# Optimization experiments

Measured on AMD Instinct MI355X. Metric: run time of the kernel, lower is better.

## Reference

```python
import jax, jax.numpy as jnp
import numpy as np

DIM = 1024
HEADS = 16
DIM_HEAD = 64
INNER = HEADS * DIM_HEAD  # 1024
B, N = 2, 2048


def setup_inputs() -> dict:
    key = jax.random.key(0)
    ks = jax.random.split(key, 6)
    x = jax.random.normal(ks[0], (B, N, DIM), dtype=jnp.float32)
    rel_pos_bias = jax.random.normal(ks[1], (1, HEADS, N, N), dtype=jnp.float32)
    g = jnp.ones((DIM,), dtype=jnp.float32)
    # Linear weights stored torch-style as [out_features, in_features].
    # Note: original zero-inits Wo; we use small random values so outputs/grads are non-trivial.
    Wq = jax.random.normal(ks[2], (INNER, DIM), dtype=jnp.float32) * (DIM ** -0.5)
    Wkv = jax.random.normal(ks[3], (2 * INNER, DIM), dtype=jnp.float32) * (DIM ** -0.5)
    Wo = jax.random.normal(ks[4], (DIM, INNER), dtype=jnp.float32) * (INNER ** -0.5)
    return {"x": x, "rel_pos_bias": rel_pos_bias, "g": g, "Wq": Wq, "Wkv": Wkv, "Wo": Wo}


def reference(x, rel_pos_bias, g, Wq, Wkv, Wo):
    eps = 1e-5  # x is float32
    # Faithful to source: normalize over dim=1 (sequence axis), biased variance.
    mean = jnp.mean(x, axis=1, keepdims=True)          # [b, 1, d]
    var = jnp.var(x, axis=1, keepdims=True)            # [b, 1, d]
    xn = (x - mean) * jax.lax.rsqrt(jnp.maximum(var, eps)) * g

    q = xn @ Wq.T                                      # [b, n, inner]
    kv = xn @ Wkv.T                                    # [b, n, 2*inner]
    k, v = jnp.split(kv, 2, axis=-1)

    def to_heads(t):  # b n (h d) -> b h n d
        b, n, _ = t.shape
        return t.reshape(b, n, HEADS, DIM_HEAD).transpose(0, 2, 1, 3)

    q, k, v = to_heads(q), to_heads(k), to_heads(v)
    q = q * (DIM_HEAD ** -0.5)

    sim = jnp.einsum('bhid,bhjd->bhij', q, k) + rel_pos_bias  # [b, h, n, n]
    attn = jax.nn.softmax(sim, axis=-1)
    out = jnp.einsum('bhij,bhjd->bhid', attn, v)              # [b, h, n, d]
    out = out.transpose(0, 2, 1, 3).reshape(x.shape[0], x.shape[1], INNER)
    return out @ Wo.T                                         # [b, n, dim]
```

## Files before the change

### kernel.cpp

```cpp
#include <hip/hip_runtime.h>
#include <hip/hip_bf16.h>

typedef __bf16 bf16;
typedef __attribute__((ext_vector_type(8))) __bf16 bf16x8;
typedef __attribute__((ext_vector_type(4))) __bf16 bf16x4;
typedef __attribute__((ext_vector_type(4))) float f32x4;
typedef __attribute__((ext_vector_type(16))) float f32x16;
typedef __attribute__((ext_vector_type(4))) unsigned int u32x4;

#define DIMD  1024
#define SEQ   2048
#define BATCH 2
#define HEADS 16
#define INNER 1024
#define QKVN  3072
#define ROWS  (BATCH*SEQ)
#define LOG2E 1.44269504f

__global__ void ln_partial(const float* __restrict__ x,
                           float* __restrict__ psum, float* __restrict__ psq) {
    const int nc = blockIdx.x;
    const int b  = blockIdx.y;
    const int t  = threadIdx.x;
    const float* xp = x + ((size_t)b*SEQ + (size_t)nc*32)*DIMD;
    float s0=0,s1=0,s2=0,s3=0,q0=0,q1=0,q2=0,q3=0;
    for (int r=0; r<32; ++r) {
        const float* row = xp + (size_t)r*DIMD;
        float v0=row[t], v1=row[t+256], v2=row[t+512], v3=row[t+768];
        s0+=v0; q0+=v0*v0; s1+=v1; q1+=v1*v1;
        s2+=v2; q2+=v2*v2; s3+=v3; q3+=v3*v3;
    }
    float* ps = psum + ((size_t)b*64 + nc)*DIMD;
    float* pq = psq  + ((size_t)b*64 + nc)*DIMD;
    ps[t]=s0; ps[t+256]=s1; ps[t+512]=s2; ps[t+768]=s3;
    pq[t]=q0; pq[t+256]=q1; pq[t+512]=q2; pq[t+768]=q3;
}

__global__ void ln_finalize(const float* __restrict__ psum, const float* __restrict__ psq,
                            const float* __restrict__ g,
                            float* __restrict__ scale, float* __restrict__ shift) {
    const int d = blockIdx.x*256 + threadIdx.x;
    const int b = blockIdx.y;
    float s=0.f, q=0.f;
    for (int nc=0; nc<64; ++nc) {
        s += psum[((size_t)b*64+nc)*DIMD + d];
        q += psq [((size_t)b*64+nc)*DIMD + d];
    }
    const float inv_n = 1.f/(float)SEQ;
    float mean = s*inv_n;
    float var  = q*inv_n - mean*mean;
    var = fmaxf(var, 1e-5f);
    scale[b*DIMD+d] = g[d]*rsqrtf(var);
    shift[b*DIMD+d] = mean;
}

__global__ void ln_apply(const float* __restrict__ x,
                         const float* __restrict__ scale, const float* __restrict__ shift,
                         bf16* __restrict__ xn) {
    size_t idx = ((size_t)blockIdx.x*256 + threadIdx.x)*4;
    int b = (int)(idx >> 21);
    int d = (int)(idx & (DIMD-1));
    f32x4 v  = *reinterpret_cast<const f32x4*>(x + idx);
    f32x4 sc = *reinterpret_cast<const f32x4*>(scale + (size_t)b*DIMD + d);
    f32x4 sh = *reinterpret_cast<const f32x4*>(shift + (size_t)b*DIMD + d);
    bf16x4 o;
    o.x = (bf16)((v.x - sh.x)*sc.x);
    o.y = (bf16)((v.y - sh.y)*sc.y);
    o.z = (bf16)((v.z - sh.z)*sc.z);
    o.w = (bf16)((v.w - sh.w)*sc.w);
    *reinterpret_cast<bf16x4*>(xn + idx) = o;
}

__global__ void castk_all(const float* __restrict__ Wq, const float* __restrict__ Wkv,
                          const float* __restrict__ Wo,
                          bf16* __restrict__ wqkv, bf16* __restrict__ wo, float qs) {
    int i = (blockIdx.x*256 + threadIdx.x)*4;
    f32x4 v; bf16* dst;
    if (i < 1048576)      { v = *reinterpret_cast<const f32x4*>(Wq + i);
                            v.x*=qs; v.y*=qs; v.z*=qs; v.w*=qs; dst = wqkv + i; }
    else if (i < 3145728) { v = *reinterpret_cast<const f32x4*>(Wkv + (i-1048576));
                            dst = wqkv + i; }
    else                  { v = *reinterpret_cast<const f32x4*>(Wo + (i-3145728));
                            dst = wo + (i-3145728); }
    bf16x4 o; o.x=(bf16)v.x; o.y=(bf16)v.y; o.z=(bf16)v.z; o.w=(bf16)v.w;
    *reinterpret_cast<bf16x4*>(dst) = o;
}

__device__ __forceinline__ void gload16(const void* g, void* l) {
    __builtin_amdgcn_global_load_lds(
        (const __attribute__((address_space(1))) unsigned int*)g,
        (__attribute__((address_space(3))) unsigned int*)l,
        16, 0, 0);
}

__device__ inline void store_out(float* p, float v) { *p = v; }
__device__ inline void store_out(bf16*  p, float v) { *p = (bf16)v; }

template <typename OT, bool FUSE_VT>
__global__ __launch_bounds__(256, 2)
void gemm_bt(const bf16* __restrict__ A, const bf16* __restrict__ B,
             OT* __restrict__ C, bf16* __restrict__ vTout, int M, int N, int K) {
    __shared__ bf16 As[128*64];
    __shared__ bf16 Bs[128*64];
    const int t = threadIdx.x;
    const int wave = t >> 6, lane = t & 63;
    const int wr = wave >> 1, wc = wave & 1;
    const int m0 = blockIdx.y*128, n0 = blockIdx.x*128;
    const int lr = lane & 15, lg = lane >> 4;
    const int srow = wave*32 + (lane>>3);
    const int scol = (lane&7)*8;

    f32x4 acc[4][4];
    #pragma unroll
    for (int i=0;i<4;++i)
        #pragma unroll
        for (int j=0;j<4;++j) acc[i][j] = (f32x4){0.f,0.f,0.f,0.f};

    for (int k0=0; k0<K; k0+=64) {
        #pragma unroll
        for (int i=0;i<4;++i) {
            gload16(A + (size_t)(m0+srow+8*i)*K + k0 + scol, As + (srow+8*i)*64 + scol);
            gload16(B + (size_t)(n0+srow+8*i)*K + k0 + scol, Bs + (srow+8*i)*64 + scol);
        }
        __syncthreads();
        #pragma unroll
        for (int kk=0; kk<2; ++kk) {
            bf16x8 a[4], b[4];
            #pragma unroll
            for (int mi=0;mi<4;++mi)
                a[mi] = *reinterpret_cast<const bf16x8*>(As + (wr*64+mi*16+lr)*64 + kk*32+lg*8);
            #pragma unroll
            for (int ni=0;ni<4;++ni)
                b[ni] = *reinterpret_cast<const bf16x8*>(Bs + (wc*64+ni*16+lr)*64 + kk*32+lg*8);
            #pragma unroll
            for (int mi=0;mi<4;++mi)
                #pragma unroll
                for (int ni=0;ni<4;++ni)
                    acc[mi][ni] = __builtin_amdgcn_mfma_f32_16x16x32_bf16(a[mi], b[ni], acc[mi][ni], 0, 0, 0);
        }
        __syncthreads();
    }
    if (FUSE_VT && n0 >= 2*INNER) {
        #pragma unroll
        for (int mi=0;mi<4;++mi)
            #pragma unroll
            for (int ni=0;ni<4;++ni) {
                int row0 = m0 + wr*64 + mi*16 + lg*4;
                int col  = n0 + wc*64 + ni*16 + lr;
                int vcol = col - 2*INNER;
                int bb = row0 >> 11, nn = row0 & (SEQ-1);
                size_t vrow = (size_t)(bb*HEADS + (vcol>>6))*64 + (vcol&63);
                bf16x4 pk;
                pk[0]=(bf16)acc[mi][ni][0]; pk[1]=(bf16)acc[mi][ni][1];
                pk[2]=(bf16)acc[mi][ni][2]; pk[3]=(bf16)acc[mi][ni][3];
                *reinterpret_cast<bf16x4*>(vTout + vrow*SEQ + nn) = pk;
            }
    } else {
        #pragma unroll
        for (int mi=0;mi<4;++mi)
            #pragma unroll
            for (int ni=0;ni<4;++ni)
                #pragma unroll
                for (int r=0;r<4;++r) {
                    int row = m0 + wr*64 + mi*16 + lg*4 + r;
                    int col = n0 + wc*64 + ni*16 + lr;
                    store_out(&C[(size_t)row*N + col], acc[mi][ni][r]);
                }
    }
}


__device__ __forceinline__ unsigned pk2(float a, float b) {
    union { bf16 h[2]; unsigned u; } x;
    x.h[0] = (bf16)a; x.h[1] = (bf16)b;
    return x.u;
}

#define ATTN_BARRIER()                                         \
    __builtin_amdgcn_sched_barrier(0);                         \
    asm volatile("s_waitcnt lgkmcnt(0)" ::: "memory");         \
    __builtin_amdgcn_s_barrier();                              \
    __builtin_amdgcn_sched_barrier(0)

#define ATTN_ITER(CUR, T)                                                          \
  {                                                                                \
              \
    if ((T)+1 < 32) {                                                              \
      *reinterpret_cast<bf16x8*>(&Ks[0][(CUR)^1][st_off])  = krA;                  \
      *reinterpret_cast<bf16x8*>(&Ks[1][(CUR)^1][st_off])  = krB;                  \
      *reinterpret_cast<bf16x8*>(&VTs[0][(CUR)^1][st_off]) = vrA;                  \
      *reinterpret_cast<bf16x8*>(&VTs[1][(CUR)^1][st_off]) = vrB;                  \
      _Pragma("unroll")                                                            \
      for (int i=0;i<4;++i)                                                        \
        *reinterpret_cast<f32x4*>(&BsL[(CUR)^1][bst[i]]) = breg[i];                \
    }                                                                              \
                      \
    if ((T)+2 < 32) {                                                              \
      krA = *reinterpret_cast<const bf16x8*>(kbase0 + (size_t)(((T)+2)*64+srow)*QKVN + scol);  \
      krB = *reinterpret_cast<const bf16x8*>(kbase1 + (size_t)(((T)+2)*64+srow)*QKVN + scol);  \
      vrA = *reinterpret_cast<const bf16x8*>(vtb0 + (size_t)srow*SEQ + ((T)+2)*64 + scol);     \
      vrB = *reinterpret_cast<const bf16x8*>(vtb1 + (size_t)srow*SEQ + ((T)+2)*64 + scol);     \
      _Pragma("unroll")                                                            \
      for (int i=0;i<4;++i)                                                        \
        breg[i] = *reinterpret_cast<const f32x4*>(bgl + (size_t)(32*i)*SEQ + ((T)+2)*64);      \
    }                                                                              \
                                    \
    f32x16 p0 = (f32x16)(0.0f), p1 = (f32x16)(0.0f);                               \
    __builtin_amdgcn_s_setprio(1);                                                 \
    _Pragma("unroll")                                                              \
    for (int s=0;s<4;++s) {                                                        \
      bf16x8 kf0 = *reinterpret_cast<const bf16x8*>(&myK[(CUR)*4096 + koff[0][s]]); \
      p0 = __builtin_amdgcn_mfma_f32_32x32x16_bf16(kf0, qf[s], p0, 0,0,0);         \
      bf16x8 kf1 = *reinterpret_cast<const bf16x8*>(&myK[(CUR)*4096 + koff[1][s]]); \
      p1 = __builtin_amdgcn_mfma_f32_32x32x16_bf16(kf1, qf[s], p1, 0,0,0);         \
    }                                                                              \
    __builtin_amdgcn_s_setprio(0);                                                 \
                              \
    f32x4 bb0[4], bb1[4];                                                          \
    _Pragma("unroll")                                                              \
    for (int rr=0;rr<4;++rr) {                                                     \
      bb0[rr] = *reinterpret_cast<const f32x4*>(&BsL[CUR][brd[0][rr]]);            \
      bb1[rr] = *reinterpret_cast<const f32x4*>(&BsL[CUR][brd[1][rr]]);            \
    }                                                                              \
            \
    float v0[16], v1[16];                                                          \
    _Pragma("unroll")                                                              \
    for (int r=0;r<16;++r) {                                                       \
      v0[r] = __builtin_fmaf(bb0[r>>2][r&3], LOG2E, p0[r]);                        \
      v1[r] = __builtin_fmaf(bb1[r>>2][r&3], LOG2E, p1[r]);                        \
    }                                                                              \
    float mx[8];                                                                   \
    _Pragma("unroll")                                                              \
    for (int i=0;i<8;++i)                                                          \
      mx[i] = fmaxf(fmaxf(v0[i], v0[i+8]), fmaxf(v1[i], v1[i+8]));                 \
    _Pragma("unroll")                                                              \
    for (int i=0;i<4;++i) mx[i] = fmaxf(mx[i], mx[i+4]);                           \
    float vmax = fmaxf(fmaxf(mx[0],mx[2]), fmaxf(mx[1],mx[3]));                    \
    vmax = fmaxf(vmax, __shfl_xor(vmax, 32));                                      \
    if (!__all(vmax <= m + 11.5f)) {                                               \
      float mnew = fmaxf(m, vmax);                                                 \
      float sc = __builtin_amdgcn_exp2f(m - mnew);                                 \
      m = mnew; l *= sc;                                                           \
      _Pragma("unroll")                                                            \
      for (int r=0;r<16;++r) {                                                     \
        float scr = __shfl(sc, (r&3)+8*(r>>2)+4*hi);                               \
        accO0[r] *= scr; accO1[r] *= scr;                                          \
      }                                                                            \
    }                                                                              \
    float e0[16], e1[16];                                                          \
    _Pragma("unroll")                                                              \
    for (int r=0;r<16;++r) {                                                       \
      e0[r] = __builtin_amdgcn_exp2f(v0[r] - m);                                   \
      e1[r] = __builtin_amdgcn_exp2f(v1[r] - m);                                   \
    }                                                                              \
    float sm[8];                                                                   \
    _Pragma("unroll")                                                              \
    for (int i=0;i<8;++i) sm[i] = (e0[i]+e0[i+8]) + (e1[i]+e1[i+8]);               \
    _Pragma("unroll")                                                              \
    for (int i=0;i<4;++i) sm[i] += sm[i+4];                                        \
    float rsum = (sm[0]+sm[2]) + (sm[1]+sm[3]);                                    \
    rsum += __shfl_xor(rsum, 32);                                                  \
    l += rsum;                                                                     \
           \
    unsigned W0[4][2], W1[4][2];                                                   \
    _Pragma("unroll")                                                              \
    for (int rr=0;rr<4;++rr) {                                                     \
      W0[rr][0] = pk2(e0[4*rr+0], e0[4*rr+1]);                                     \
      W0[rr][1] = pk2(e0[4*rr+2], e0[4*rr+3]);                                     \
      W1[rr][0] = pk2(e1[4*rr+0], e1[4*rr+1]);                                     \
      W1[rr][1] = pk2(e1[4*rr+2], e1[4*rr+3]);                                     \
    }                                                                              \
                               \
    bf16x8 pa[4];                                                                  \
    _Pragma("unroll")                                                              \
    for (int s4=0;s4<4;++s4) {                                                     \
      unsigned u[4];                                                               \
      _Pragma("unroll")                                                            \
      for (int hh=0;hh<2;++hh) {                                                   \
        unsigned a0 = (s4>>1) ? W1[2*(s4&1)  ][hh] : W0[2*(s4&1)  ][hh];           \
        unsigned a1 = (s4>>1) ? W1[2*(s4&1)+1][hh] : W0[2*(s4&1)+1][hh];           \
        unsigned X = hi ? a0 : a1;                                                 \
        unsigned R = (unsigned)__shfl_xor((int)X, 32);                             \
        u[hh]   = hi ? R  : a0;                                                    \
        u[2+hh] = hi ? a1 : R;                                                     \
      }                                                                            \
      u32x4 uv = {u[0], u[1], u[2], u[3]};                                         \
      pa[s4] = __builtin_bit_cast(bf16x8, uv);                                     \
    }                                                                              \
                                                                        \
    __builtin_amdgcn_s_setprio(1);                                                 \
    _Pragma("unroll")                                                              \
    for (int s4=0;s4<4;++s4) {                                                     \
      bf16x8 vfa = *reinterpret_cast<const bf16x8*>(&myV[(CUR)*4096 + voff[0][s4]]); \
      accO0 = __builtin_amdgcn_mfma_f32_32x32x16_bf16(pa[s4], vfa, accO0, 0,0,0);  \
      bf16x8 vfb = *reinterpret_cast<const bf16x8*>(&myV[(CUR)*4096 + voff[1][s4]]); \
      accO1 = __builtin_amdgcn_mfma_f32_32x32x16_bf16(pa[s4], vfb, accO1, 0,0,0);  \
    }                                                                              \
    __builtin_amdgcn_s_setprio(0);                                                 \
    ATTN_BARRIER();                                                                \
  }

__global__ __launch_bounds__(512, 1)
void attn_kernel(const bf16* __restrict__ qkv, const bf16* __restrict__ vTg,
                 const float* __restrict__ bias, bf16* __restrict__ oh) {
    __shared__ bf16 Ks[2][2][64*64];
    __shared__ bf16 VTs[2][2][64*64];
    __shared__ float BsL[2][128*64];

    const int qt = blockIdx.x, h = blockIdx.y;
    const int t = threadIdx.x;
    const int w = t >> 6, lane = t & 63;
    const int wb = w >> 2;
    const int wq = w & 3;
    const int ql = lane & 31, hi = lane >> 5;
    const int q0 = qt*128;

    int koff[2][4], voff[2][4];
    #pragma unroll
    for (int B2=0;B2<2;++B2)
        #pragma unroll
        for (int s=0;s<4;++s) {
            koff[B2][s] = (32*B2+ql)*64 + (((2*s+hi) ^ (ql&7))*8);
            voff[B2][s] = (32*B2+ql)*64 + (((2*s+hi) ^ (ql&7))*8);
        }
    bf16* myK = (bf16*)Ks[wb];
    bf16* myV = (bf16*)VTs[wb];

    int bst[4];
    {
        int rlow = t>>4;
        int swg  = ((t&15) ^ (rlow&15))*4;
        #pragma unroll
        for (int i=0;i<4;++i)
            bst[i] = (32*i + rlow)*64 + swg;
    }
    int brd[2][4];
    #pragma unroll
    for (int B2=0;B2<2;++B2)
        #pragma unroll
        for (int rr=0;rr<4;++rr)
            brd[B2][rr] = (wq*32+ql)*64 + (((8*B2+2*rr+hi) ^ (ql&15))*4);

    const int srow = t>>3;
    const int scol = (t&7)*8;
    const int st_off = srow*64 + (((t&7) ^ (srow&7))*8);

    const bf16* qrow = qkv + ((size_t)(wb*SEQ + q0 + wq*32 + ql))*QKVN + h*64 + hi*8;
    bf16x8 qf[4];
    #pragma unroll
    for (int s=0;s<4;++s)
        qf[s] = *reinterpret_cast<const bf16x8*>(qrow + 16*s);

    const bf16* kbase0 = qkv + INNER + h*64;
    const bf16* kbase1 = qkv + (size_t)SEQ*QKVN + INNER + h*64;
    const bf16* vtb0   = vTg + (size_t)h*64*SEQ;
    const bf16* vtb1   = vTg + (size_t)(HEADS + h)*64*SEQ;
    const float* bgl = bias + ((size_t)h*SEQ + (size_t)(q0 + (t>>4)))*SEQ + 4*(t&15);

    bf16x8 krA, krB, vrA, vrB;
    f32x4 breg[4];

    *reinterpret_cast<bf16x8*>(&Ks[0][0][st_off]) =
        *reinterpret_cast<const bf16x8*>(kbase0 + (size_t)srow*QKVN + scol);
    *reinterpret_cast<bf16x8*>(&Ks[1][0][st_off]) =
        *reinterpret_cast<const bf16x8*>(kbase1 + (size_t)srow*QKVN + scol);
    *reinterpret_cast<bf16x8*>(&VTs[0][0][st_off]) =
        *reinterpret_cast<const bf16x8*>(vtb0 + (size_t)srow*SEQ + scol);
    *reinterpret_cast<bf16x8*>(&VTs[1][0][st_off]) =
        *reinterpret_cast<const bf16x8*>(vtb1 + (size_t)srow*SEQ + scol);
    #pragma unroll
    for (int i=0;i<4;++i)
        breg[i] = *reinterpret_cast<const f32x4*>(bgl + (size_t)(32*i)*SEQ);
    #pragma unroll
    for (int i=0;i<4;++i)
        *reinterpret_cast<f32x4*>(&BsL[0][bst[i]]) = breg[i];
    krA = *reinterpret_cast<const bf16x8*>(kbase0 + (size_t)(64+srow)*QKVN + scol);
    krB = *reinterpret_cast<const bf16x8*>(kbase1 + (size_t)(64+srow)*QKVN + scol);
    vrA = *reinterpret_cast<const bf16x8*>(vtb0 + (size_t)srow*SEQ + 64 + scol);
    vrB = *reinterpret_cast<const bf16x8*>(vtb1 + (size_t)srow*SEQ + 64 + scol);
    #pragma unroll
    for (int i=0;i<4;++i)
        breg[i] = *reinterpret_cast<const f32x4*>(bgl + (size_t)(32*i)*SEQ + 64);
    ATTN_BARRIER();

    float m = -__builtin_inff();
    float l = 0.f;
    f32x16 accO0 = (f32x16)(0.0f), accO1 = (f32x16)(0.0f);

    for (int t2 = 0; t2 < 32; t2 += 2) {
        ATTN_ITER(0, t2);
        ATTN_ITER(1, t2+1);
    }

    float linv = 1.f/l;
    bf16* ob = oh + ((size_t)(wb*SEQ + q0 + wq*32))*INNER + h*64 + ql;
    #pragma unroll
    for (int r=0;r<16;++r) {
        int qoff = (r&3) + 8*(r>>2) + 4*hi;
        float li = __shfl(linv, qoff);
        ob[(size_t)qoff*INNER]      = (bf16)(accO0[r]*li);
        ob[(size_t)qoff*INNER + 32] = (bf16)(accO1[r]*li);
    }
}

extern "C" void kernel_launch(void* const* d_in, const int* in_sizes, int n_in,
                              void* d_out, int out_size, void* d_ws, size_t ws_size,
                              hipStream_t stream) {
    const float* x    = (const float*)d_in[0];
    const float* bias = (const float*)d_in[1];
    const float* g    = (const float*)d_in[2];
    const float* Wq   = (const float*)d_in[3];
    const float* Wkv  = (const float*)d_in[4];
    const float* Wo   = (const float*)d_in[5];
    float* out = (float*)d_out;

    char* ws = (char*)d_ws;
    bf16*  xn    = (bf16*)(ws);
    bf16*  vT    = (bf16*)(ws + 8388608);
    bf16*  wqkv  = (bf16*)(ws + 16777216);
    bf16*  wo    = (bf16*)(ws + 23068672);
    bf16*  qkv   = (bf16*)(ws + 25165824);
    bf16*  oh    = (bf16*)(ws + 50331648);
    float* psum  = (float*)(ws + 58720256);
    float* psq   = (float*)(ws + 59244544);
    float* scale = (float*)(ws + 59768832);
    float* shift = (float*)(ws + 59777024);

    ln_partial <<<dim3(64,2), 256, 0, stream>>>(x, psum, psq);
    ln_finalize<<<dim3(4,2),  256, 0, stream>>>(psum, psq, g, scale, shift);
    ln_apply   <<<dim3(4096), 256, 0, stream>>>(x, scale, shift, xn);

    castk_all<<<dim3(4096), 256, 0, stream>>>(Wq, Wkv, Wo, wqkv, wo, 0.125f*LOG2E);

    gemm_bt<bf16,true><<<dim3(24,32), 256, 0, stream>>>(xn, wqkv, qkv, vT, ROWS, QKVN, DIMD);

    attn_kernel<<<dim3(16,16), 512, 0, stream>>>(qkv, vT, bias, oh);

    gemm_bt<float,false><<<dim3(8,32), 256, 0, stream>>>(oh, wo, out, nullptr, ROWS, INNER, INNER);
}
```

Before: 172.0 us.

## Switch attention K/V/bias staging to direct global-to-LDS loads with triple buffering

Staging of K, V and bias tiles in the attention loop changes from register-staged loads plus LDS stores to direct global-to-LDS loads (gload16). The pre-swizzled source addresses keep the existing LDS layout. K/V get a three-deep buffer ring with loads issued two tiles ahead, and bias is double-buffered one tile ahead. Waits use partial vmcnt counts so loads stay in flight across the barrier. This removes VGPR staging and LDS write instructions from the loop and deepens prefetch, at the cost of more LDS and careful counter-based synchronisation that can race if the counts are wrong.

```diff
diff --git a/kernel.cpp b/kernel.cpp
--- a/kernel.cpp
+++ b/kernel.cpp
@@ -176,51 +176,40 @@
     return x.u;
 }
 
-#define ATTN_BARRIER()                                         \
-    __builtin_amdgcn_sched_barrier(0);                         \
-    asm volatile("s_waitcnt lgkmcnt(0)" ::: "memory");         \
-    __builtin_amdgcn_s_barrier();                              \
-    __builtin_amdgcn_sched_barrier(0)
-
-#define ATTN_ITER(CUR, T)                                                          \
+#define ATTN_ITER(KB, KW, BB, BW, T, TAIL)                                         \
   {                                                                                \
-              \
-    if ((T)+1 < 32) {                                                              \
-      *reinterpret_cast<bf16x8*>(&Ks[0][(CUR)^1][st_off])  = krA;                  \
-      *reinterpret_cast<bf16x8*>(&Ks[1][(CUR)^1][st_off])  = krB;                  \
-      *reinterpret_cast<bf16x8*>(&VTs[0][(CUR)^1][st_off]) = vrA;                  \
-      *reinterpret_cast<bf16x8*>(&VTs[1][(CUR)^1][st_off]) = vrB;                  \
+                         \
+    if (!(TAIL) || (T)+1 < 32) {                                                   \
       _Pragma("unroll")                                                            \
-      for (int i=0;i<4;++i)                                                        \
-        *reinterpret_cast<f32x4*>(&BsL[(CUR)^1][bst[i]]) = breg[i];                \
-    }                                                                              \
-                      \
-    if ((T)+2 < 32) {                                                              \
-      krA = *reinterpret_cast<const bf16x8*>(kbase0 + (size_t)(((T)+2)*64+srow)*QKVN + scol);  \
-      krB = *reinterpret_cast<const bf16x8*>(kbase1 + (size_t)(((T)+2)*64+srow)*QKVN + scol);  \
-      vrA = *reinterpret_cast<const bf16x8*>(vtb0 + (size_t)srow*SEQ + ((T)+2)*64 + scol);     \
-      vrB = *reinterpret_cast<const bf16x8*>(vtb1 + (size_t)srow*SEQ + ((T)+2)*64 + scol);     \
-      _Pragma("unroll")                                                            \
-      for (int i=0;i<4;++i)                                                        \
-        breg[i] = *reinterpret_cast<const f32x4*>(bgl + (size_t)(32*i)*SEQ + ((T)+2)*64);      \
-    }                                                                              \
+      for (int i_=0;i_<4;++i_)                                                     \
+        gload16(bptr + (size_t)(32*i_)*SEQ + ((T)+1)*64, &BsL[BW][t*4 + i_*2048]); \
+    }                                                                              \
+    __builtin_amdgcn_sched_barrier(0);                                             \
+                                                 \
+    if (!(TAIL) || (T)+2 < 32) {                                                   \
+      gload16(kA + (size_t)((T)+2)*64*QKVN, &Ks[0][KW][t*8]);                      \
+      gload16(kB + (size_t)((T)+2)*64*QKVN, &Ks[1][KW][t*8]);                      \
+      gload16(vA + ((T)+2)*64,              &VTs[0][KW][t*8]);                     \
+      gload16(vB + ((T)+2)*64,              &VTs[1][KW][t*8]);                     \
+    }                                                                              \
+    __builtin_amdgcn_sched_barrier(0);                                             \
                                     \
     f32x16 p0 = (f32x16)(0.0f), p1 = (f32x16)(0.0f);                               \
     __builtin_amdgcn_s_setprio(1);                                                 \
     _Pragma("unroll")                                                              \
     for (int s=0;s<4;++s) {                                                        \
-      bf16x8 kf0 = *reinterpret_cast<const bf16x8*>(&myK[(CUR)*4096 + koff[0][s]]); \
+      bf16x8 kf0 = *reinterpret_cast<const bf16x8*>(&myK[(KB)*4096 + koff[0][s]]); \
       p0 = __builtin_amdgcn_mfma_f32_32x32x16_bf16(kf0, qf[s], p0, 0,0,0);         \
-      bf16x8 kf1 = *reinterpret_cast<const bf16x8*>(&myK[(CUR)*4096 + koff[1][s]]); \
+      bf16x8 kf1 = *reinterpret_cast<const bf16x8*>(&myK[(KB)*4096 + koff[1][s]]); \
       p1 = __builtin_amdgcn_mfma_f32_32x32x16_bf16(kf1, qf[s], p1, 0,0,0);         \
     }                                                                              \
     __builtin_amdgcn_s_setprio(0);                                                 \
-                              \
+                                       \
     f32x4 bb0[4], bb1[4];                                                          \
     _Pragma("unroll")                                                              \
     for (int rr=0;rr<4;++rr) {                                                     \
-      bb0[rr] = *reinterpret_cast<const f32x4*>(&BsL[CUR][brd[0][rr]]);            \
-      bb1[rr] = *reinterpret_cast<const f32x4*>(&BsL[CUR][brd[1][rr]]);            \
+      bb0[rr] = *reinterpret_cast<const f32x4*>(&BsL[BB][brd[0][rr]]);             \
+      bb1[rr] = *reinterpret_cast<const f32x4*>(&BsL[BB][brd[1][rr]]);             \
     }                                                                              \
             \
     float v0[16], v1[16];                                                          \
@@ -291,21 +280,26 @@
     __builtin_amdgcn_s_setprio(1);                                                 \
     _Pragma("unroll")                                                              \
     for (int s4=0;s4<4;++s4) {                                                     \
-      bf16x8 vfa = *reinterpret_cast<const bf16x8*>(&myV[(CUR)*4096 + voff[0][s4]]); \
+      bf16x8 vfa = *reinterpret_cast<const bf16x8*>(&myV[(KB)*4096 + voff[0][s4]]); \
       accO0 = __builtin_amdgcn_mfma_f32_32x32x16_bf16(pa[s4], vfa, accO0, 0,0,0);  \
-      bf16x8 vfb = *reinterpret_cast<const bf16x8*>(&myV[(CUR)*4096 + voff[1][s4]]); \
+      bf16x8 vfb = *reinterpret_cast<const bf16x8*>(&myV[(KB)*4096 + voff[1][s4]]); \
       accO1 = __builtin_amdgcn_mfma_f32_32x32x16_bf16(pa[s4], vfb, accO1, 0,0,0);  \
     }                                                                              \
     __builtin_amdgcn_s_setprio(0);                                                 \
-    ATTN_BARRIER();                                                                \
+             \
+    __builtin_amdgcn_sched_barrier(0);                                             \
+    if (TAIL) { asm volatile("s_waitcnt vmcnt(0) lgkmcnt(0)" ::: "memory"); }      \
+    else      { asm volatile("s_waitcnt vmcnt(4) lgkmcnt(0)" ::: "memory"); }      \
+    __builtin_amdgcn_s_barrier();                                                  \
+    __builtin_amdgcn_sched_barrier(0);                                             \
   }
 
 __global__ __launch_bounds__(512, 1)
 void attn_kernel(const bf16* __restrict__ qkv, const bf16* __restrict__ vTg,
                  const float* __restrict__ bias, bf16* __restrict__ oh) {
-    __shared__ bf16 Ks[2][2][64*64];
-    __shared__ bf16 VTs[2][2][64*64];
-    __shared__ float BsL[2][128*64];
+    __shared__ bf16 Ks[2][3][4096];
+    __shared__ bf16 VTs[2][3][4096];
+    __shared__ float BsL[2][8192];
 
     const int qt = blockIdx.x, h = blockIdx.y;
     const int t = threadIdx.x;
@@ -326,14 +320,6 @@
     bf16* myK = (bf16*)Ks[wb];
     bf16* myV = (bf16*)VTs[wb];
 
-    int bst[4];
-    {
-        int rlow = t>>4;
-        int swg  = ((t&15) ^ (rlow&15))*4;
-        #pragma unroll
-        for (int i=0;i<4;++i)
-            bst[i] = (32*i + rlow)*64 + swg;
-    }
     int brd[2][4];
     #pragma unroll
     for (int B2=0;B2<2;++B2)
@@ -341,56 +327,56 @@
         for (int rr=0;rr<4;++rr)
             brd[B2][rr] = (wq*32+ql)*64 + (((8*B2+2*rr+hi) ^ (ql&15))*4);
 
-    const int srow = t>>3;
-    const int scol = (t&7)*8;
-    const int st_off = srow*64 + (((t&7) ^ (srow&7))*8);
-
-    const bf16* qrow = qkv + ((size_t)(wb*SEQ + q0 + wq*32 + ql))*QKVN + h*64 + hi*8;
-    bf16x8 qf[4];
-    #pragma unroll
-    for (int s=0;s<4;++s)
-        qf[s] = *reinterpret_cast<const bf16x8*>(qrow + 16*s);
-
+    const int swz8k = (((t&7) ^ ((t>>3)&7))*8);
     const bf16* kbase0 = qkv + INNER + h*64;
     const bf16* kbase1 = qkv + (size_t)SEQ*QKVN + INNER + h*64;
     const bf16* vtb0   = vTg + (size_t)h*64*SEQ;
     const bf16* vtb1   = vTg + (size_t)(HEADS + h)*64*SEQ;
-    const float* bgl = bias + ((size_t)h*SEQ + (size_t)(q0 + (t>>4)))*SEQ + 4*(t&15);
-
-    bf16x8 krA, krB, vrA, vrB;
-    f32x4 breg[4];
-
-    *reinterpret_cast<bf16x8*>(&Ks[0][0][st_off]) =
-        *reinterpret_cast<const bf16x8*>(kbase0 + (size_t)srow*QKVN + scol);
-    *reinterpret_cast<bf16x8*>(&Ks[1][0][st_off]) =
-        *reinterpret_cast<const bf16x8*>(kbase1 + (size_t)srow*QKVN + scol);
-    *reinterpret_cast<bf16x8*>(&VTs[0][0][st_off]) =
-        *reinterpret_cast<const bf16x8*>(vtb0 + (size_t)srow*SEQ + scol);
-    *reinterpret_cast<bf16x8*>(&VTs[1][0][st_off]) =
-        *reinterpret_cast<const bf16x8*>(vtb1 + (size_t)srow*SEQ + scol);
-    #pragma unroll
-    for (int i=0;i<4;++i)
-        breg[i] = *reinterpret_cast<const f32x4*>(bgl + (size_t)(32*i)*SEQ);
-    #pragma unroll
-    for (int i=0;i<4;++i)
-        *reinterpret_cast<f32x4*>(&BsL[0][bst[i]]) = breg[i];
-    krA = *reinterpret_cast<const bf16x8*>(kbase0 + (size_t)(64+srow)*QKVN + scol);
-    krB = *reinterpret_cast<const bf16x8*>(kbase1 + (size_t)(64+srow)*QKVN + scol);
-    vrA = *reinterpret_cast<const bf16x8*>(vtb0 + (size_t)srow*SEQ + 64 + scol);
-    vrB = *reinterpret_cast<const bf16x8*>(vtb1 + (size_t)srow*SEQ + 64 + scol);
-    #pragma unroll
-    for (int i=0;i<4;++i)
-        breg[i] = *reinterpret_cast<const f32x4*>(bgl + (size_t)(32*i)*SEQ + 64);
-    ATTN_BARRIER();
+    const bf16* kA = kbase0 + (size_t)(t>>3)*QKVN + swz8k;
+    const bf16* kB = kbase1 + (size_t)(t>>3)*QKVN + swz8k;
+    const bf16* vA = vtb0 + (size_t)(t>>3)*SEQ + swz8k;
+    const bf16* vB = vtb1 + (size_t)(t>>3)*SEQ + swz8k;
+    const float* bptr = bias + ((size_t)h*SEQ + (size_t)(q0 + (t>>4)))*SEQ
+                              + (((t&15) ^ ((t>>4)&15))*4);
+
+    const bf16* qrow = qkv + ((size_t)(wb*SEQ + q0 + wq*32 + ql))*QKVN + h*64 + hi*8;
+    bf16x8 qf[4];
+    #pragma unroll
+    for (int s=0;s<4;++s)
+        qf[s] = *reinterpret_cast<const bf16x8*>(qrow + 16*s);
+
+    #pragma unroll
+    for (int i_=0;i_<4;++i_)
+        gload16(bptr + (size_t)(32*i_)*SEQ, &BsL[0][t*4 + i_*2048]);
+    __builtin_amdgcn_sched_barrier(0);
+    gload16(kA,                    &Ks[0][0][t*8]);
+    gload16(kB,                    &Ks[1][0][t*8]);
+    gload16(vA,                    &VTs[0][0][t*8]);
+    gload16(vB,                    &VTs[1][0][t*8]);
+    __builtin_amdgcn_sched_barrier(0);
+    gload16(kA + (size_t)64*QKVN,  &Ks[0][1][t*8]);
+    gload16(kB + (size_t)64*QKVN,  &Ks[1][1][t*8]);
+    gload16(vA + 64,               &VTs[0][1][t*8]);
+    gload16(vB + 64,               &VTs[1][1][t*8]);
+    __builtin_amdgcn_sched_barrier(0);
+    asm volatile("s_waitcnt vmcnt(4) lgkmcnt(0)" ::: "memory");
+    __builtin_amdgcn_s_barrier();
+    __builtin_amdgcn_sched_barrier(0);
 
     float m = -__builtin_inff();
     float l = 0.f;
     f32x16 accO0 = (f32x16)(0.0f), accO1 = (f32x16)(0.0f);
 
-    for (int t2 = 0; t2 < 32; t2 += 2) {
-        ATTN_ITER(0, t2);
-        ATTN_ITER(1, t2+1);
-    }
+    for (int t6 = 0; t6 < 30; t6 += 6) {
+        ATTN_ITER(0,2,0,1, t6+0, 0);
+        ATTN_ITER(1,0,1,0, t6+1, 0);
+        ATTN_ITER(2,1,0,1, t6+2, 0);
+        ATTN_ITER(0,2,1,0, t6+3, 0);
+        ATTN_ITER(1,0,0,1, t6+4, 0);
+        ATTN_ITER(2,1,1,0, t6+5, 0);
+    }
+    ATTN_ITER(0,2,0,1, 30, 1);
+    ATTN_ITER(1,0,1,0, 31, 1);
 
     float linv = 1.f/l;
     bf16* ob = oh + ((size_t)(wb*SEQ + q0 + wq*32))*INNER + h*64 + ql;
```

Measured after the change: 193.0 us. 1.12x slower.
